# Optimization experiments

Measured on AMD Instinct MI355X. Metric: run time of the kernel, lower is better.

Reference implementation:

```python
import jax, jax.numpy as jnp
import numpy as np

B, N, C = 4, 2048, 768
H = 12
D = C // H  # head_dim = 64


def setup_inputs() -> dict:
    key = jax.random.key(0)
    k1, k2, k3, k4, k5 = jax.random.split(key, 5)
    s = 0.02
    return {
        "x": jax.random.normal(k1, (B, N, C), dtype=jnp.float32),
        "qkv_w": jax.random.normal(k2, (3 * C, C), dtype=jnp.float32) * s,
        "qkv_b": jax.random.normal(k3, (3 * C,), dtype=jnp.float32) * s,
        "proj_w": jax.random.normal(k4, (C, C), dtype=jnp.float32) * s,
        "proj_b": jax.random.normal(k5, (C,), dtype=jnp.float32) * s,
    }


def reference(x, qkv_w, qkv_b, proj_w, proj_b):
    b, n, c = x.shape
    # qkv projection (torch Linear: x @ W.T + b) -> [B,N,3,H,D] -> [3,B,H,N,D]
    qkv = (x @ qkv_w.T + qkv_b).reshape(b, n, 3, H, D).transpose(2, 0, 3, 1, 4)
    q, k, v = qkv[0], qkv[1], qkv[2]
    scale = D ** (-0.5)
    attn = jnp.einsum("bhqd,bhkd->bhqk", q, k) * scale
    attn = jax.nn.softmax(attn, axis=-1)
    # dropout is identity in eval mode
    out = jnp.einsum("bhqk,bhkd->bhqd", attn, v)  # [B,H,N,D]
    out = out.transpose(0, 2, 1, 3).reshape(b, n, c)
    return out @ proj_w.T + proj_b
```

## Files before the change

### kernel.cpp

```cpp
#include <hip/hip_runtime.h>
#include <hip/hip_bf16.h>
#include <stdint.h>

typedef __bf16 bf16_t;
typedef __bf16 bf16x8 __attribute__((ext_vector_type(8)));
typedef float f32x4 __attribute__((ext_vector_type(4)));

#define NB 4
#define NH 12
#define ND 64
#define NN 2048
#define NC 768

__device__ __forceinline__ void async_copy16(const bf16_t* g, bf16_t* l) {
    __builtin_amdgcn_global_load_lds((__attribute__((address_space(1))) void*)(void*)g,
                                     (__attribute__((address_space(3))) void*)l, 16, 0, 0);
}

__global__ void cast_kernel(const float* __restrict__ src, bf16_t* __restrict__ dst, int n4) {
    int i = blockIdx.x * blockDim.x + threadIdx.x;
    if (i >= n4) return;
    float4 v = ((const float4*)src)[i];
    union { bf16_t e[4]; uint2 u; } t;
    t.e[0] = (bf16_t)v.x; t.e[1] = (bf16_t)v.y; t.e[2] = (bf16_t)v.z; t.e[3] = (bf16_t)v.w;
    ((uint2*)dst)[i] = t.u;
}

__device__ __forceinline__ int vperm(int s) {
    return (s & 32) | (((s >> 2) & 3) << 3) | (((s >> 4) & 1) << 2) | (s & 3);
}


__launch_bounds__(256)
__global__ void qkv_gemm_kernel(const bf16_t* __restrict__ X, const bf16_t* __restrict__ W,
                                const float* __restrict__ bias,
                                bf16_t* __restrict__ Q, bf16_t* __restrict__ K, bf16_t* __restrict__ V)
{
    __shared__ __align__(16) bf16_t sA[128 * 64];
    __shared__ __align__(16) bf16_t sB[128 * 64];
    const int tid  = threadIdx.x;
    const int lane = tid & 63;
    const int w    = tid >> 6;
    const int wm   = w & 1, wn = w >> 1;
    const int m0   = blockIdx.x * 128;
    const int n0   = blockIdx.y * 128;
    const int lrow = lane & 15;
    const int quad = lane >> 4;
    const int arow = lane >> 3;
    const int gch  = (lane & 7) ^ arow;

    f32x4 zero = {0.f, 0.f, 0.f, 0.f};
    f32x4 acc[4][4];
#pragma unroll
    for (int i = 0; i < 4; ++i)
#pragma unroll
        for (int j = 0; j < 4; ++j) acc[i][j] = zero;

    for (int kt = 0; kt < NC; kt += 64) {
        __syncthreads();
        for (int c = w; c < 16; c += 4) {
            async_copy16(X + (size_t)(m0 + c * 8 + arow) * NC + kt + gch * 8, sA + c * 512);
            async_copy16(W + (size_t)(n0 + c * 8 + arow) * NC + kt + gch * 8, sB + c * 512);
        }
        __syncthreads();
#pragma unroll
        for (int h = 0; h < 2; ++h) {
            bf16x8 af[4], bfr[4];
#pragma unroll
            for (int i = 0; i < 4; ++i) {
                int r = wm * 64 + i * 16 + lrow;
                af[i] = *(const bf16x8*)(sA + r * 64 + (((h * 4 + quad) ^ (r & 7)) * 8));
            }
#pragma unroll
            for (int j = 0; j < 4; ++j) {
                int r = wn * 64 + j * 16 + lrow;
                bfr[j] = *(const bf16x8*)(sB + r * 64 + (((h * 4 + quad) ^ (r & 7)) * 8));
            }
#pragma unroll
            for (int i = 0; i < 4; ++i)
#pragma unroll
                for (int j = 0; j < 4; ++j)
                    acc[i][j] = __builtin_amdgcn_mfma_f32_16x16x32_bf16(af[i], bfr[j], acc[i][j], 0, 0, 0);
        }
    }

    const int colbase = n0 + wn * 64;
    const int t3 = colbase / NC;
    const int h  = (colbase % NC) / ND;
    const float qscale = 0.125f * 1.44269504088896340736f;

#pragma unroll
    for (int j = 0; j < 4; ++j) {
        const int d  = j * 16 + lrow;
        const float bv = bias[colbase + d];
#pragma unroll
        for (int i = 0; i < 4; ++i) {
            const int rowg = m0 + wm * 64 + i * 16 + quad * 4;
            const int bb = rowg >> 11;
            const int nn = rowg & 2047;
            if (t3 == 2) {
                union { bf16_t e[4]; uint2 u; } pk;
#pragma unroll
                for (int p = 0; p < 4; ++p) pk.e[p] = (bf16_t)(acc[i][j][p] + bv);
                const int pos = (nn & ~63) | vperm(nn & 63);
                *(uint2*)(V + ((size_t)(bb * NH + h) * ND + d) * NN + pos) = pk.u;
            } else {
                bf16_t* outb = t3 ? K : Q;
#pragma unroll
                for (int p = 0; p < 4; ++p) {
                    float val = acc[i][j][p] + bv;
                    if (t3 == 0) val *= qscale;
                    outb[((size_t)(bb * NH + h) * NN + nn + p) * ND + d] = (bf16_t)val;
                }
            }
        }
    }
}

__launch_bounds__(512)
__global__ void attn_kernel(const bf16_t* __restrict__ Q, const bf16_t* __restrict__ K,
                            const bf16_t* __restrict__ Vt, bf16_t* __restrict__ O)
{
    __shared__ __align__(16) bf16_t sQ[128 * 64];
    __shared__ __align__(16) bf16_t sK[64 * 64];
    __shared__ __align__(16) bf16_t sV[64 * 64];
    const int tid  = threadIdx.x;
    const int lane = tid & 63;
    const int w    = tid >> 6;
    const int qt   = blockIdx.x;
    const int h    = blockIdx.y;
    const int b    = blockIdx.z;
    const int lrow = lane & 15;
    const int quad = lane >> 4;
    const int arow = lane >> 3;
    const int gch  = (lane & 7) ^ arow;
    const size_t head_off = (size_t)(b * NH + h) * NN * ND;
    const bf16_t* qh = Q  + head_off;
    const bf16_t* kh = K  + head_off;
    const bf16_t* vh = Vt + head_off;

    for (int c = w; c < 16; c += 8)
        async_copy16(qh + (size_t)(qt * 128 + c * 8 + arow) * ND + gch * 8, sQ + c * 512);
    __syncthreads();

    bf16x8 qb[2];
#pragma unroll
    for (int hh = 0; hh < 2; ++hh)
        qb[hh] = *(const bf16x8*)(sQ + (w * 16 + lrow) * 64 + (((hh * 4 + quad) ^ (lrow & 7)) * 8));

    f32x4 zero = {0.f, 0.f, 0.f, 0.f};
    f32x4 o[4];
#pragma unroll
    for (int db = 0; db < 4; ++db) o[db] = zero;
    float l_i = 0.f;

    for (int it = 0; it < NN / 64; ++it) {
        __syncthreads();
        const bf16_t* kb = kh + (size_t)it * 64 * ND;
        async_copy16(kb + (size_t)(w * 8 + arow) * ND + gch * 8, sK + w * 512);
        async_copy16(vh + (size_t)(w * 8 + arow) * NN + it * 64 + gch * 8, sV + w * 512);
        __syncthreads();

        f32x4 s[4];
#pragma unroll
        for (int blk = 0; blk < 4; ++blk) {
            int r = blk * 16 + lrow;
            bf16x8 a0 = *(const bf16x8*)(sK + r * 64 + ((quad ^ (r & 7)) * 8));
            bf16x8 a1 = *(const bf16x8*)(sK + r * 64 + (((4 + quad) ^ (r & 7)) * 8));
            f32x4 z = zero;
            z = __builtin_amdgcn_mfma_f32_16x16x32_bf16(a0, qb[0], z, 0, 0, 0);
            z = __builtin_amdgcn_mfma_f32_16x16x32_bf16(a1, qb[1], z, 0, 0, 0);
            s[blk] = z;
        }

        union { bf16_t e[16]; bf16x8 v[2]; } pe;
        float rs = 0.f;
#pragma unroll
        for (int blk = 0; blk < 4; ++blk)
#pragma unroll
            for (int p = 0; p < 4; ++p) {
                float ev = exp2f(s[blk][p]);
                rs += ev;
                pe.e[(blk >> 1) * 8 + (blk & 1) * 4 + p] = (bf16_t)ev;
            }
        rs += __shfl_xor(rs, 16);
        rs += __shfl_xor(rs, 32);
        l_i += rs;

#pragma unroll
        for (int db = 0; db < 4; ++db) {
            int r = db * 16 + lrow;
            bf16x8 v0 = *(const bf16x8*)(sV + r * 64 + ((quad ^ (r & 7)) * 8));
            bf16x8 v1 = *(const bf16x8*)(sV + r * 64 + (((4 + quad) ^ (r & 7)) * 8));
            o[db] = __builtin_amdgcn_mfma_f32_16x16x32_bf16(v0, pe.v[0], o[db], 0, 0, 0);
            o[db] = __builtin_amdgcn_mfma_f32_16x16x32_bf16(v1, pe.v[1], o[db], 0, 0, 0);
        }
    }

    const float rl = 1.0f / l_i;
    const int n = qt * 128 + w * 16 + lrow;
    const size_t rowoff = ((size_t)(b * NN + n)) * NC + h * ND;
#pragma unroll
    for (int db = 0; db < 4; ++db) {
        union { bf16_t e[4]; uint2 u; } pk;
#pragma unroll
        for (int p = 0; p < 4; ++p) pk.e[p] = (bf16_t)(o[db][p] * rl);
        *(uint2*)(O + rowoff + db * 16 + quad * 4) = pk.u;
    }
}

__launch_bounds__(256)
__global__ void proj_gemm_kernel(const bf16_t* __restrict__ A, const bf16_t* __restrict__ W,
                                 const float* __restrict__ bias, float* __restrict__ out)
{
    __shared__ __align__(16) bf16_t sA[128 * 64];
    __shared__ __align__(16) bf16_t sB[128 * 64];
    const int tid  = threadIdx.x;
    const int lane = tid & 63;
    const int w    = tid >> 6;
    const int wm   = w & 1, wn = w >> 1;
    const int m0   = blockIdx.x * 128;
    const int n0   = blockIdx.y * 128;
    const int lrow = lane & 15;
    const int quad = lane >> 4;
    const int arow = lane >> 3;
    const int gch  = (lane & 7) ^ arow;

    f32x4 zero = {0.f, 0.f, 0.f, 0.f};
    f32x4 acc[4][4];
#pragma unroll
    for (int i = 0; i < 4; ++i)
#pragma unroll
        for (int j = 0; j < 4; ++j) acc[i][j] = zero;

    for (int kt = 0; kt < NC; kt += 64) {
        __syncthreads();
        for (int c = w; c < 16; c += 4) {
            async_copy16(A + (size_t)(m0 + c * 8 + arow) * NC + kt + gch * 8, sA + c * 512);
            async_copy16(W + (size_t)(n0 + c * 8 + arow) * NC + kt + gch * 8, sB + c * 512);
        }
        __syncthreads();
#pragma unroll
        for (int h = 0; h < 2; ++h) {
            bf16x8 af[4], bfr[4];
#pragma unroll
            for (int i = 0; i < 4; ++i) {
                int r = wm * 64 + i * 16 + lrow;
                af[i] = *(const bf16x8*)(sA + r * 64 + (((h * 4 + quad) ^ (r & 7)) * 8));
            }
#pragma unroll
            for (int j = 0; j < 4; ++j) {
                int r = wn * 64 + j * 16 + lrow;
                bfr[j] = *(const bf16x8*)(sB + r * 64 + (((h * 4 + quad) ^ (r & 7)) * 8));
            }
#pragma unroll
            for (int i = 0; i < 4; ++i)
#pragma unroll
                for (int j = 0; j < 4; ++j)
                    acc[i][j] = __builtin_amdgcn_mfma_f32_16x16x32_bf16(af[i], bfr[j], acc[i][j], 0, 0, 0);
        }
    }

#pragma unroll
    for (int j = 0; j < 4; ++j) {
        const int colg = n0 + wn * 64 + j * 16 + lrow;
        const float bv = bias[colg];
#pragma unroll
        for (int i = 0; i < 4; ++i) {
            const int rowg = m0 + wm * 64 + i * 16 + quad * 4;
#pragma unroll
            for (int p = 0; p < 4; ++p)
                out[(size_t)(rowg + p) * NC + colg] = acc[i][j][p] + bv;
        }
    }
}

extern "C" void kernel_launch(void* const* d_in, const int* in_sizes, int n_in,
                              void* d_out, int out_size, void* d_ws, size_t ws_size,
                              hipStream_t stream) {
    const float* x      = (const float*)d_in[0];
    const float* qkv_w  = (const float*)d_in[1];
    const float* qkv_b  = (const float*)d_in[2];
    const float* proj_w = (const float*)d_in[3];
    const float* proj_b = (const float*)d_in[4];
    float* out = (float*)d_out;

    char* ws = (char*)d_ws;
    bf16_t* xb    = (bf16_t*)ws; ws += (size_t)8192 * 768 * 2;
    bf16_t* wqkv  = (bf16_t*)ws; ws += (size_t)2304 * 768 * 2;
    bf16_t* wproj = (bf16_t*)ws; ws += (size_t)768 * 768 * 2;
    bf16_t* qb    = (bf16_t*)ws; ws += (size_t)NB * NH * NN * ND * 2;
    bf16_t* kb    = (bf16_t*)ws; ws += (size_t)NB * NH * NN * ND * 2;
    bf16_t* vb    = (bf16_t*)ws; ws += (size_t)NB * NH * NN * ND * 2;
    bf16_t* ab    = (bf16_t*)ws; ws += (size_t)8192 * 768 * 2;

    cast_kernel<<<(8192 * 768 / 4 + 255) / 256, 256, 0, stream>>>(x, xb, 8192 * 768 / 4);
    cast_kernel<<<(2304 * 768 / 4 + 255) / 256, 256, 0, stream>>>(qkv_w, wqkv, 2304 * 768 / 4);
    cast_kernel<<<(768 * 768 / 4 + 255) / 256, 256, 0, stream>>>(proj_w, wproj, 768 * 768 / 4);

    qkv_gemm_kernel<<<dim3(8192 / 128, 2304 / 128), 256, 0, stream>>>(xb, wqkv, qkv_b, qb, kb, vb);
    attn_kernel<<<dim3(NN / 128, NH, NB), 512, 0, stream>>>(qb, kb, vb, ab);
    proj_gemm_kernel<<<dim3(8192 / 128, 768 / 128), 256, 0, stream>>>(ab, wproj, proj_b, out);
}
```

Baseline: 229.3 us.

## Swap MFMA operands for vectorized epilogue stores and double K/V tile per sync

In the QKV and projection GEMMs the MFMA operands are swapped for Q/K and output tiles, so each lane holds 4 consecutive columns. The epilogue can then issue 8-byte bf16 or 16-byte float4 stores and a float4 bias load instead of scattered scalar stores. The V path keeps the original orientation for its transposed layout. The attention kernel loads two 64-key K/V tiles per barrier pair, halving synchronisations, and defers the row-sum cross-lane shuffles to the end. This doubles K/V shared memory and adds a runtime branch on t3 in the GEMM inner loop.

Measured after the change: 234.9 us. +2.5%, slower.

```diff
diff --git a/kernel.cpp b/kernel.cpp
--- a/kernel.cpp
+++ b/kernel.cpp
@@ -49,6 +49,10 @@
     const int arow = lane >> 3;
     const int gch  = (lane & 7) ^ arow;
 
+    const int colbase = n0 + wn * 64;
+    const int t3 = colbase / NC;
+    const int h  = (colbase % NC) / ND;
+
     f32x4 zero = {0.f, 0.f, 0.f, 0.f};
     f32x4 acc[4][4];
 #pragma unroll
@@ -64,54 +68,72 @@
         }
         __syncthreads();
 #pragma unroll
-        for (int h = 0; h < 2; ++h) {
-            bf16x8 af[4], bfr[4];
+        for (int hh = 0; hh < 2; ++hh) {
+            bf16x8 xf[4], wf[4];
 #pragma unroll
             for (int i = 0; i < 4; ++i) {
                 int r = wm * 64 + i * 16 + lrow;
-                af[i] = *(const bf16x8*)(sA + r * 64 + (((h * 4 + quad) ^ (r & 7)) * 8));
+                xf[i] = *(const bf16x8*)(sA + r * 64 + (((hh * 4 + quad) ^ (r & 7)) * 8));
             }
 #pragma unroll
             for (int j = 0; j < 4; ++j) {
                 int r = wn * 64 + j * 16 + lrow;
-                bfr[j] = *(const bf16x8*)(sB + r * 64 + (((h * 4 + quad) ^ (r & 7)) * 8));
-            }
-#pragma unroll
-            for (int i = 0; i < 4; ++i)
-#pragma unroll
-                for (int j = 0; j < 4; ++j)
-                    acc[i][j] = __builtin_amdgcn_mfma_f32_16x16x32_bf16(af[i], bfr[j], acc[i][j], 0, 0, 0);
-        }
-    }
-
-    const int colbase = n0 + wn * 64;
-    const int t3 = colbase / NC;
-    const int h  = (colbase % NC) / ND;
+                wf[j] = *(const bf16x8*)(sB + r * 64 + (((hh * 4 + quad) ^ (r & 7)) * 8));
+            }
+            if (t3 < 2) {
+#pragma unroll
+                for (int i = 0; i < 4; ++i)
+#pragma unroll
+                    for (int j = 0; j < 4; ++j)
+                        acc[i][j] = __builtin_amdgcn_mfma_f32_16x16x32_bf16(wf[j], xf[i], acc[i][j], 0, 0, 0);
+            } else {
+#pragma unroll
+                for (int i = 0; i < 4; ++i)
+#pragma unroll
+                    for (int j = 0; j < 4; ++j)
+                        acc[i][j] = __builtin_amdgcn_mfma_f32_16x16x32_bf16(xf[i], wf[j], acc[i][j], 0, 0, 0);
+            }
+        }
+    }
+
     const float qscale = 0.125f * 1.44269504088896340736f;
 
-#pragma unroll
-    for (int j = 0; j < 4; ++j) {
-        const int d  = j * 16 + lrow;
-        const float bv = bias[colbase + d];
-#pragma unroll
-        for (int i = 0; i < 4; ++i) {
-            const int rowg = m0 + wm * 64 + i * 16 + quad * 4;
-            const int bb = rowg >> 11;
-            const int nn = rowg & 2047;
-            if (t3 == 2) {
+    if (t3 < 2) {
+        bf16_t* outb = t3 ? K : Q;
+#pragma unroll
+        for (int j = 0; j < 4; ++j) {
+            const int dcol = j * 16 + quad * 4;
+            const float4 bv4 = *(const float4*)(bias + colbase + dcol);
+#pragma unroll
+            for (int i = 0; i < 4; ++i) {
+                const int tok = m0 + wm * 64 + i * 16 + lrow;
+                const int bb = tok >> 11;
+                const int nn = tok & 2047;
+                union { bf16_t e[4]; uint2 u; } pk;
+#pragma unroll
+                for (int p = 0; p < 4; ++p) {
+                    float val = acc[i][j][p] + (&bv4.x)[p];
+                    if (t3 == 0) val *= qscale;
+                    pk.e[p] = (bf16_t)val;
+                }
+                *(uint2*)(outb + ((size_t)(bb * NH + h) * NN + nn) * ND + dcol) = pk.u;
+            }
+        }
+    } else {
+#pragma unroll
+        for (int j = 0; j < 4; ++j) {
+            const int d  = j * 16 + lrow;
+            const float bv = bias[colbase + d];
+#pragma unroll
+            for (int i = 0; i < 4; ++i) {
+                const int tok0 = m0 + wm * 64 + i * 16 + quad * 4;
+                const int bb = tok0 >> 11;
+                const int nn = tok0 & 2047;
                 union { bf16_t e[4]; uint2 u; } pk;
 #pragma unroll
                 for (int p = 0; p < 4; ++p) pk.e[p] = (bf16_t)(acc[i][j][p] + bv);
                 const int pos = (nn & ~63) | vperm(nn & 63);
                 *(uint2*)(V + ((size_t)(bb * NH + h) * ND + d) * NN + pos) = pk.u;
-            } else {
-                bf16_t* outb = t3 ? K : Q;
-#pragma unroll
-                for (int p = 0; p < 4; ++p) {
-                    float val = acc[i][j][p] + bv;
-                    if (t3 == 0) val *= qscale;
-                    outb[((size_t)(bb * NH + h) * NN + nn + p) * ND + d] = (bf16_t)val;
-                }
             }
         }
     }
@@ -122,8 +144,8 @@
                             const bf16_t* __restrict__ Vt, bf16_t* __restrict__ O)
 {
     __shared__ __align__(16) bf16_t sQ[128 * 64];
-    __shared__ __align__(16) bf16_t sK[64 * 64];
-    __shared__ __align__(16) bf16_t sV[64 * 64];
+    __shared__ __align__(16) bf16_t sK[2][64 * 64];
+    __shared__ __align__(16) bf16_t sV[2][64 * 64];
     const int tid  = threadIdx.x;
     const int lane = tid & 63;
     const int w    = tid >> 6;
@@ -154,50 +176,64 @@
     for (int db = 0; db < 4; ++db) o[db] = zero;
     float l_i = 0.f;
 
-    for (int it = 0; it < NN / 64; ++it) {
-        __syncthreads();
-        const bf16_t* kb = kh + (size_t)it * 64 * ND;
-        async_copy16(kb + (size_t)(w * 8 + arow) * ND + gch * 8, sK + w * 512);
-        async_copy16(vh + (size_t)(w * 8 + arow) * NN + it * 64 + gch * 8, sV + w * 512);
-        __syncthreads();
-
-        f32x4 s[4];
-#pragma unroll
-        for (int blk = 0; blk < 4; ++blk) {
-            int r = blk * 16 + lrow;
-            bf16x8 a0 = *(const bf16x8*)(sK + r * 64 + ((quad ^ (r & 7)) * 8));
-            bf16x8 a1 = *(const bf16x8*)(sK + r * 64 + (((4 + quad) ^ (r & 7)) * 8));
-            f32x4 z = zero;
-            z = __builtin_amdgcn_mfma_f32_16x16x32_bf16(a0, qb[0], z, 0, 0, 0);
-            z = __builtin_amdgcn_mfma_f32_16x16x32_bf16(a1, qb[1], z, 0, 0, 0);
-            s[blk] = z;
-        }
-
-        union { bf16_t e[16]; bf16x8 v[2]; } pe;
-        float rs = 0.f;
-#pragma unroll
-        for (int blk = 0; blk < 4; ++blk)
-#pragma unroll
-            for (int p = 0; p < 4; ++p) {
-                float ev = exp2f(s[blk][p]);
-                rs += ev;
-                pe.e[(blk >> 1) * 8 + (blk & 1) * 4 + p] = (bf16_t)ev;
-            }
-        rs += __shfl_xor(rs, 16);
-        rs += __shfl_xor(rs, 32);
-        l_i += rs;
-
-#pragma unroll
-        for (int db = 0; db < 4; ++db) {
-            int r = db * 16 + lrow;
-            bf16x8 v0 = *(const bf16x8*)(sV + r * 64 + ((quad ^ (r & 7)) * 8));
-            bf16x8 v1 = *(const bf16x8*)(sV + r * 64 + (((4 + quad) ^ (r & 7)) * 8));
-            o[db] = __builtin_amdgcn_mfma_f32_16x16x32_bf16(v0, pe.v[0], o[db], 0, 0, 0);
-            o[db] = __builtin_amdgcn_mfma_f32_16x16x32_bf16(v1, pe.v[1], o[db], 0, 0, 0);
-        }
-    }
-
+    const bf16_t* kbase = kh + (size_t)(w * 8 + arow) * ND + gch * 8;
+    const bf16_t* vbase = vh + (size_t)(w * 8 + arow) * NN + gch * 8;
+
+    for (int it = 0; it < NN / 128; ++it) {
+        __syncthreads();
+        async_copy16(kbase + (size_t)(it * 128) * ND,      sK[0] + w * 512);
+        async_copy16(kbase + (size_t)(it * 128 + 64) * ND, sK[1] + w * 512);
+        async_copy16(vbase + it * 128,                     sV[0] + w * 512);
+        async_copy16(vbase + it * 128 + 64,                sV[1] + w * 512);
+        __syncthreads();
+
+#pragma unroll
+        for (int half = 0; half < 2; ++half) {
+            const bf16_t* sKh = sK[half];
+            const bf16_t* sVh = sV[half];
+            f32x4 s[4];
+#pragma unroll
+            for (int blk = 0; blk < 4; ++blk) {
+                int r = blk * 16 + lrow;
+                bf16x8 a0 = *(const bf16x8*)(sKh + r * 64 + ((quad ^ (r & 7)) * 8));
+                bf16x8 a1 = *(const bf16x8*)(sKh + r * 64 + (((4 + quad) ^ (r & 7)) * 8));
+                f32x4 z = zero;
+                z = __builtin_amdgcn_mfma_f32_16x16x32_bf16(a0, qb[0], z, 0, 0, 0);
+                z = __builtin_amdgcn_mfma_f32_16x16x32_bf16(a1, qb[1], z, 0, 0, 0);
+                s[blk] = z;
+            }
+
+            union { __hip_bfloat162 h2[8]; bf16x8 v[2]; } pe;
+            float rs0 = 0.f, rs1 = 0.f;
+#pragma unroll
+            for (int blk = 0; blk < 4; ++blk) {
+                float e0 = exp2f(s[blk][0]);
+                float e1 = exp2f(s[blk][1]);
+                float e2 = exp2f(s[blk][2]);
+                float e3 = exp2f(s[blk][3]);
+                rs0 += e0 + e1;
+                rs1 += e2 + e3;
+                const int hb = (blk >> 1) * 4 + (blk & 1) * 2;
+                pe.h2[hb]     = __float22bfloat162_rn(make_float2(e0, e1));
+                pe.h2[hb + 1] = __float22bfloat162_rn(make_float2(e2, e3));
+            }
+            l_i += rs0 + rs1;
+
+#pragma unroll
+            for (int db = 0; db < 4; ++db) {
+                int r = db * 16 + lrow;
+                bf16x8 v0 = *(const bf16x8*)(sVh + r * 64 + ((quad ^ (r & 7)) * 8));
+                bf16x8 v1 = *(const bf16x8*)(sVh + r * 64 + (((4 + quad) ^ (r & 7)) * 8));
+                o[db] = __builtin_amdgcn_mfma_f32_16x16x32_bf16(v0, pe.v[0], o[db], 0, 0, 0);
+                o[db] = __builtin_amdgcn_mfma_f32_16x16x32_bf16(v1, pe.v[1], o[db], 0, 0, 0);
+            }
+        }
+    }
+
+    l_i += __shfl_xor(l_i, 16);
+    l_i += __shfl_xor(l_i, 32);
     const float rl = 1.0f / l_i;
+
     const int n = qt * 128 + w * 16 + lrow;
     const size_t rowoff = ((size_t)(b * NN + n)) * NC + h * ND;
 #pragma unroll
@@ -241,36 +277,37 @@
         }
         __syncthreads();
 #pragma unroll
-        for (int h = 0; h < 2; ++h) {
-            bf16x8 af[4], bfr[4];
+        for (int hh = 0; hh < 2; ++hh) {
+            bf16x8 xf[4], wf[4];
 #pragma unroll
             for (int i = 0; i < 4; ++i) {
                 int r = wm * 64 + i * 16 + lrow;
-                af[i] = *(const bf16x8*)(sA + r * 64 + (((h * 4 + quad) ^ (r & 7)) * 8));
+                xf[i] = *(const bf16x8*)(sA + r * 64 + (((hh * 4 + quad) ^ (r & 7)) * 8));
             }
 #pragma unroll
             for (int j = 0; j < 4; ++j) {
                 int r = wn * 64 + j * 16 + lrow;
-                bfr[j] = *(const bf16x8*)(sB + r * 64 + (((h * 4 + quad) ^ (r & 7)) * 8));
+                wf[j] = *(const bf16x8*)(sB + r * 64 + (((hh * 4 + quad) ^ (r & 7)) * 8));
             }
 #pragma unroll
             for (int i = 0; i < 4; ++i)
 #pragma unroll
                 for (int j = 0; j < 4; ++j)
-                    acc[i][j] = __builtin_amdgcn_mfma_f32_16x16x32_bf16(af[i], bfr[j], acc[i][j], 0, 0, 0);
+                    acc[i][j] = __builtin_amdgcn_mfma_f32_16x16x32_bf16(wf[j], xf[i], acc[i][j], 0, 0, 0);
         }
     }
 
 #pragma unroll
     for (int j = 0; j < 4; ++j) {
-        const int colg = n0 + wn * 64 + j * 16 + lrow;
-        const float bv = bias[colg];
+        const int colg0 = n0 + wn * 64 + j * 16 + quad * 4;
+        const float4 bv4 = *(const float4*)(bias + colg0);
 #pragma unroll
         for (int i = 0; i < 4; ++i) {
-            const int rowg = m0 + wm * 64 + i * 16 + quad * 4;
-#pragma unroll
-            for (int p = 0; p < 4; ++p)
-                out[(size_t)(rowg + p) * NC + colg] = acc[i][j][p] + bv;
+            const int tok = m0 + wm * 64 + i * 16 + lrow;
+            float4 val;
+#pragma unroll
+            for (int p = 0; p < 4; ++p) (&val.x)[p] = acc[i][j][p] + (&bv4.x)[p];
+            *(float4*)(out + (size_t)tok * NC + colg0) = val;
         }
     }
 }
```
